# Kernel optimization log

Measured on AMD Instinct MI355X. Metric: run time of the kernel, lower is better.

## Reference

```python
import jax, jax.numpy as jnp
import numpy as np

DIM = 192
HEADS = 8
EPS = 1e-12  # torch F.normalize eps


def _l2norm(t):
    # normalize over last axis, matching torch.nn.functional.normalize
    n = jnp.sqrt(jnp.sum(t * t, axis=-1, keepdims=True))
    return t / jnp.maximum(n, EPS)


def setup_inputs() -> dict:
    key = jax.random.key(0)
    k1, k2, k3, k4 = jax.random.split(key, 4)
    B, C, H, W = 16, DIM, 128, 128
    s = 1.0 / np.sqrt(C)
    return {
        "x": jax.random.normal(k1, (B, C, H, W), dtype=jnp.float32),
        "w_qkv": jax.random.normal(k2, (C, 3 * C), dtype=jnp.float32) * s,
        "w_proj": jax.random.normal(k3, (C, C), dtype=jnp.float32) * s,
        "b_proj": jax.random.normal(k4, (C,), dtype=jnp.float32) * 0.01,
        "temperature": jnp.ones((HEADS, 1, 1), dtype=jnp.float32),
    }


def reference(x, w_qkv, w_proj, b_proj, temperature):
    B, C, H, W = x.shape
    N = H * W
    h = HEADS
    d = C // h
    # [B,C,H,W] -> [B,N,C]
    xt = x.reshape(B, C, N).transpose(0, 2, 1)
    qkv = (xt @ w_qkv).reshape(B, N, 3, h, d)
    qkv = qkv.transpose(2, 0, 3, 1, 4)           # [3,B,h,N,d]
    q, k, v = qkv[0], qkv[1], qkv[2]
    # transpose to channel-as-token: [B,h,d,N]
    q = _l2norm(q.transpose(0, 1, 3, 2))
    k = _l2norm(k.transpose(0, 1, 3, 2))
    v = v.transpose(0, 1, 3, 2)
    # small channel attention matrix [B,h,d,d]
    attn = jnp.einsum("bhdn,bhen->bhde", q, k) * temperature
    attn = jax.nn.softmax(attn, axis=-1)
    out = jnp.einsum("bhde,bhen->bhdn", attn, v)  # [B,h,d,N]
    out = out.transpose(0, 3, 1, 2).reshape(B, N, C)
    out = out @ w_proj + b_proj
    return out.transpose(0, 2, 1).reshape(B, C, H, W)
```

## Files before the change

kernel.cpp:

```cpp
#include <hip/hip_runtime.h>
#include <hip/hip_bf16.h>
#include <math.h>

#define C_DIM 192
#define NTOK 16384
#define NB 16
#define NH 8
#define HD 24
#define EPSN 1e-12f

typedef float f32x4 __attribute__((ext_vector_type(4)));
typedef __bf16 bf16x4 __attribute__((ext_vector_type(4)));
typedef __bf16 bf16x8 __attribute__((ext_vector_type(8)));

__device__ __forceinline__ f32x4 mfma16(bf16x8 a, bf16x8 b, f32x4 c) {
  return __builtin_amdgcn_mfma_f32_16x16x32_bf16(a, b, c, 0, 0, 0);
}

__device__ __forceinline__ bf16x8 cvt8(const float* __restrict__ p) {
  f32x4 a = *(const f32x4*)p;
  f32x4 b = *(const f32x4*)(p + 4);
  bf16x8 r;
  r[0] = (__bf16)a[0]; r[1] = (__bf16)a[1]; r[2] = (__bf16)a[2]; r[3] = (__bf16)a[3];
  r[4] = (__bf16)b[0]; r[5] = (__bf16)b[1]; r[6] = (__bf16)b[2]; r[7] = (__bf16)b[3];
  return r;
}

__global__ __launch_bounds__(256, 2) void k1_gram(const float* __restrict__ x,
                                                  float* __restrict__ gpart,
                                                  int kc) {
  const int b = blockIdx.y, chunk = blockIdx.x;
  const float* xb = x + (size_t)b * C_DIM * NTOK + (size_t)chunk * kc;
  __shared__ __bf16 xsh[2][C_DIM * 32];
  const int t = threadIdx.x;
  const int lane = t & 63, wid = t >> 6;
  const int lrow = lane & 15, loct = lane >> 4;
  const int r0 = (wid >> 1) * 96, c0 = (wid & 1) * 96;
  f32x4 acc[6][6] = {};
  f32x4 stg[6];

#pragma unroll
  for (int it = 0; it < 6; ++it) {
    int idx = it * 256 + t, r = idx >> 3, c8 = idx & 7;
    stg[it] = *(const f32x4*)(xb + (size_t)r * NTOK + 4 * c8);
  }
#pragma unroll
  for (int it = 0; it < 6; ++it) {
    int idx = it * 256 + t, r = idx >> 3, c8 = idx & 7;
    bf16x4 w;
    w[0] = (__bf16)stg[it][0]; w[1] = (__bf16)stg[it][1];
    w[2] = (__bf16)stg[it][2]; w[3] = (__bf16)stg[it][3];
    *(bf16x4*)(&xsh[0][r * 32 + 4 * c8]) = w;
  }
  __syncthreads();

  for (int ks = 0; ks < kc; ks += 32) {
    const int cur = (ks >> 5) & 1;
    const bool more = (ks + 32) < kc;
    if (more) {
#pragma unroll
      for (int it = 0; it < 6; ++it) {
        int idx = it * 256 + t, r = idx >> 3, c8 = idx & 7;
        stg[it] = *(const f32x4*)(xb + (size_t)r * NTOK + ks + 32 + 4 * c8);
      }
    }
    bf16x8 fa[6];
#pragma unroll
    for (int i = 0; i < 6; ++i)
      fa[i] = *(const bf16x8*)(&xsh[cur][(r0 + 16 * i + lrow) * 32 + 8 * loct]);
#pragma unroll
    for (int j = 0; j < 6; ++j) {
      bf16x8 fb = *(const bf16x8*)(&xsh[cur][(c0 + 16 * j + lrow) * 32 + 8 * loct]);
#pragma unroll
      for (int i = 0; i < 6; ++i) acc[i][j] = mfma16(fa[i], fb, acc[i][j]);
    }
    if (more) {
#pragma unroll
      for (int it = 0; it < 6; ++it) {
        int idx = it * 256 + t, r = idx >> 3, c8 = idx & 7;
        bf16x4 w;
        w[0] = (__bf16)stg[it][0]; w[1] = (__bf16)stg[it][1];
        w[2] = (__bf16)stg[it][2]; w[3] = (__bf16)stg[it][3];
        *(bf16x4*)(&xsh[cur ^ 1][r * 32 + 4 * c8]) = w;
      }
    }
    __syncthreads();
  }
  float* gp = gpart + ((size_t)chunk * NB + b) * C_DIM * C_DIM;
#pragma unroll
  for (int i = 0; i < 6; ++i)
#pragma unroll
    for (int j = 0; j < 6; ++j)
#pragma unroll
      for (int e = 0; e < 4; ++e)
        gp[(size_t)(r0 + 16 * i + 4 * loct + e) * C_DIM + (c0 + 16 * j + lrow)] =
            acc[i][j][e];
}

__global__ __launch_bounds__(256) void k2a_reduce(const float* __restrict__ gpart,
                                                  float* __restrict__ G,
                                                  int nchunk) {
  const size_t total = (size_t)NB * C_DIM * C_DIM;
  size_t e0 = ((size_t)blockIdx.x * 256 + threadIdx.x) * 4;
  f32x4 s = {};
  for (int c = 0; c < nchunk; ++c) s += *(const f32x4*)(gpart + c * total + e0);
  *(f32x4*)(G + e0) = s;
}

__global__ __launch_bounds__(256) void k2b1_t(const float* __restrict__ G,
                                              const float* __restrict__ wqkv,
                                              float* __restrict__ Tt) {
  const int b = blockIdx.y, rb = blockIdx.x;
  const int lane = threadIdx.x & 63, wid = threadIdx.x >> 6;
  const int lrow = lane & 15, loct = lane >> 4;
  const float* Gb = G + (size_t)b * C_DIM * C_DIM;
  const int ddA = rb * 64 + wid * 16 + lrow;
  f32x4 acc[12] = {};
  for (int s = 0; s < 6; ++s) {
    bf16x8 fa;
#pragma unroll
    for (int e = 0; e < 8; ++e)
      fa[e] = (__bf16)wqkv[(size_t)(32 * s + 8 * loct + e) * 576 + ddA];
#pragma unroll
    for (int j = 0; j < 12; ++j) {
      bf16x8 fb = cvt8(Gb + (size_t)(16 * j + lrow) * C_DIM + 32 * s + 8 * loct);
      acc[j] = mfma16(fa, fb, acc[j]);
    }
  }
  float* To = Tt + (size_t)b * 384 * C_DIM;
#pragma unroll
  for (int j = 0; j < 12; ++j)
#pragma unroll
    for (int e = 0; e < 4; ++e)
      To[(size_t)(rb * 64 + wid * 16 + 4 * loct + e) * C_DIM + 16 * j + lrow] =
          acc[j][e];
}

__global__ __launch_bounds__(256) void k2b2_attn(const float* __restrict__ Tt,
                                                 const float* __restrict__ wqkv,
                                                 const float* __restrict__ temp,
                                                 float* __restrict__ Yt) {
  const int b = blockIdx.y, h = blockIdx.x;
  __shared__ float SL[32][33];
  __shared__ float qn2L[HD], kn2L[HD];
  const int t = threadIdx.x;
  const int lane = t & 63, wid = t >> 6;
  const int lrow = lane & 15, loct = lane >> 4;
  const float* Tb = Tt + (size_t)b * 384 * C_DIM;
  const int r = wid >> 1, j = wid & 1;
  f32x4 acc = {};
  for (int s = 0; s < 6; ++s) {
    bf16x8 fa = cvt8(Tb + (size_t)(h * HD + 16 * r + lrow) * C_DIM + 32 * s + 8 * loct);
    bf16x8 fb;
#pragma unroll
    for (int e = 0; e < 8; ++e)
      fb[e] = (__bf16)wqkv[(size_t)(32 * s + 8 * loct + e) * 576 + 192 + h * HD +
                           16 * j + lrow];
    acc = mfma16(fa, fb, acc);
  }
#pragma unroll
  for (int e = 0; e < 4; ++e) {
    int d = 16 * r + 4 * loct + e, ee = 16 * j + lrow;
    if (d < HD && ee < HD) SL[d][ee] = acc[e];
  }
  if (t < 48) {
    const int dd = (t < 24) ? t : t - 24;
    const int row = ((t < 24) ? 0 : 192) + h * HD + dd;
    float s = 0.f;
    for (int c = 0; c < C_DIM; ++c)
      s += Tb[(size_t)row * C_DIM + c] * wqkv[(size_t)c * 576 + row];
    if (t < 24) qn2L[dd] = s; else kn2L[dd] = s;
  }
  __syncthreads();
  if (t < HD) {
    const float tp = temp[h];
    float nq = fmaxf(sqrtf(fmaxf(qn2L[t], 0.f)), EPSN);
    float lg[HD];
    float m = -1e30f;
#pragma unroll
    for (int e = 0; e < HD; ++e) {
      float nk = fmaxf(sqrtf(fmaxf(kn2L[e], 0.f)), EPSN);
      lg[e] = SL[t][e] / (nq * nk) * tp;
      m = fmaxf(m, lg[e]);
    }
    float sum = 0.f;
#pragma unroll
    for (int e = 0; e < HD; ++e) { lg[e] = __expf(lg[e] - m); sum += lg[e]; }
    float inv = 1.f / sum;
#pragma unroll
    for (int e = 0; e < HD; ++e) SL[t][e] = lg[e] * inv;
  }
  __syncthreads();
  if (t < C_DIM) {
    float wv[HD];
#pragma unroll
    for (int e = 0; e < HD; ++e)
      wv[e] = wqkv[(size_t)t * 576 + 384 + h * HD + e];
    float* Yo = Yt + ((size_t)b * C_DIM + t) * C_DIM + h * HD;
#pragma unroll
    for (int d = 0; d < HD; ++d) {
      float y = 0.f;
#pragma unroll
      for (int e = 0; e < HD; ++e) y += SL[d][e] * wv[e];
      Yo[d] = y;
    }
  }
}

__global__ __launch_bounds__(256) void k2c_m(const float* __restrict__ wproj,
                                             const float* __restrict__ Yt,
                                             __bf16* __restrict__ M) {
  const int b = blockIdx.y, rb = blockIdx.x;
  const int lane = threadIdx.x & 63, wid = threadIdx.x >> 6;
  const int lrow = lane & 15, loct = lane >> 4;
  const float* Yb = Yt + (size_t)b * C_DIM * C_DIM;
  const int coA = rb * 64 + wid * 16 + lrow;
  f32x4 acc[12] = {};
  for (int s = 0; s < 6; ++s) {
    bf16x8 fa;
#pragma unroll
    for (int e = 0; e < 8; ++e)
      fa[e] = (__bf16)wproj[(size_t)(32 * s + 8 * loct + e) * C_DIM + coA];
#pragma unroll
    for (int j = 0; j < 12; ++j) {
      bf16x8 fb = cvt8(Yb + (size_t)(16 * j + lrow) * C_DIM + 32 * s + 8 * loct);
      acc[j] = mfma16(fa, fb, acc[j]);
    }
  }
  __bf16* Mo = M + (size_t)b * C_DIM * C_DIM;
#pragma unroll
  for (int j = 0; j < 12; ++j)
#pragma unroll
    for (int e = 0; e < 4; ++e)
      Mo[(size_t)(rb * 64 + wid * 16 + 4 * loct + e) * C_DIM + 16 * j + lrow] =
          (__bf16)acc[j][e];
}

__global__ __launch_bounds__(256, 4) void k3_out(const float* __restrict__ x,
                                                 const __bf16* __restrict__ M,
                                                 const float* __restrict__ bproj,
                                                 float* __restrict__ out) {
  const int nt = blockIdx.x, half = blockIdx.y, b = blockIdx.z;
  const int rbase = half * 96;
  __shared__ __bf16 Ml[96 * C_DIM];
  __shared__ float biasL[96];
  const __bf16* Mb = M + (size_t)b * C_DIM * C_DIM + (size_t)rbase * C_DIM;
  for (int i = threadIdx.x; i < 96 * 24; i += 256) {
    int row = i / 24, ch = i % 24;
    bf16x8 v = *(const bf16x8*)(Mb + row * C_DIM + ch * 8);
    *(bf16x8*)(Ml + row * C_DIM + ((ch ^ (row & 7)) * 8)) = v;
  }
  if (threadIdx.x < 96) biasL[threadIdx.x] = bproj[rbase + threadIdx.x];
  __syncthreads();
  const int lane = threadIdx.x & 63, wid = threadIdx.x >> 6;
  const int lrow = lane & 15, loct = lane >> 4;
  const float* xb = x + (size_t)b * C_DIM * NTOK;
  float* ob = out + (size_t)b * C_DIM * NTOK;
  const int n0 = nt * 128 + wid * 32;
  f32x4 acc[6][2] = {};
#pragma unroll
  for (int s = 0; s < 6; ++s) {
    bf16x8 fb0, fb1;
#pragma unroll
    for (int e = 0; e < 8; ++e) {
      size_t rowoff = (size_t)(32 * s + 8 * loct + e) * NTOK;
      fb0[e] = (__bf16)xb[rowoff + n0 + lrow];
      fb1[e] = (__bf16)xb[rowoff + n0 + 16 + lrow];
    }
#pragma unroll
    for (int tt = 0; tt < 6; ++tt) {
      int rowb = 16 * tt + lrow;
      bf16x8 fa = *(const bf16x8*)(Ml + rowb * C_DIM +
                                   (((4 * s + loct) ^ (rowb & 7)) * 8));
      acc[tt][0] = mfma16(fa, fb0, acc[tt][0]);
      acc[tt][1] = mfma16(fa, fb1, acc[tt][1]);
    }
  }
#pragma unroll
  for (int tt = 0; tt < 6; ++tt) {
    const int rw = 16 * tt + 4 * loct;
    f32x4 bias = *(const f32x4*)(biasL + rw);
#pragma unroll
    for (int e = 0; e < 4; ++e) {
      ob[(size_t)(rbase + rw + e) * NTOK + n0 + lrow] = acc[tt][0][e] + bias[e];
      ob[(size_t)(rbase + rw + e) * NTOK + n0 + 16 + lrow] = acc[tt][1][e] + bias[e];
    }
  }
}

extern "C" void kernel_launch(void* const* d_in, const int* in_sizes, int n_in,
                              void* d_out, int out_size, void* d_ws, size_t ws_size,
                              hipStream_t stream) {
  const float* x = (const float*)d_in[0];
  const float* wqkv = (const float*)d_in[1];
  const float* wproj = (const float*)d_in[2];
  const float* bproj = (const float*)d_in[3];
  const float* temp = (const float*)d_in[4];
  float* out = (float*)d_out;

  const size_t GSZ = (size_t)NB * C_DIM * C_DIM;
  const size_t TSZ = (size_t)NB * 384 * C_DIM;
  int nchunk = 32;
  while (nchunk > 1 &&
         ((size_t)nchunk * GSZ + GSZ + TSZ + GSZ + GSZ) * 4 > ws_size)
    nchunk >>= 1;
  float* wsf = (float*)d_ws;
  float* gpart = wsf;
  float* G = gpart + (size_t)nchunk * GSZ;
  float* Tt = G + GSZ;
  float* Yt = Tt + TSZ;
  __bf16* M = (__bf16*)(Yt + GSZ);

  k1_gram<<<dim3(nchunk, NB), 256, 0, stream>>>(x, gpart, NTOK / nchunk);
  k2a_reduce<<<dim3(576), 256, 0, stream>>>(gpart, G, nchunk);
  k2b1_t<<<dim3(6, NB), 256, 0, stream>>>(G, wqkv, Tt);
  k2b2_attn<<<dim3(NH, NB), 256, 0, stream>>>(Tt, wqkv, temp, Yt);
  k2c_m<<<dim3(3, NB), 256, 0, stream>>>(wproj, Yt, M);
  k3_out<<<dim3(128, 2, NB), 256, 0, stream>>>(x, M, bproj, out);
}
```

Baseline: 232.6 us.

## Pad gram LDS rows and restructure output GEMM to read x once

The gram kernel's shared tile row stride is padded from 32 to 40 bf16 elements, which should cut LDS bank conflicts on the MFMA fragment loads. The output kernel is rebuilt so each block covers all 192 output channels for 64 tokens. Previously two blocks each covered half the channels, so x was read twice. M fragments are now read straight from global memory instead of being staged in LDS. The next x slice is prefetched into registers, and the epilogue goes through an LDS transpose to issue 16-byte coalesced stores. This trades heavier M traffic through the cache, and more registers, for half the x reads and wider writes.

New measurement: 275.5 us. 18.4% more time.

```diff
diff --git a/kernel.cpp b/kernel.cpp
--- a/kernel.cpp
+++ b/kernel.cpp
@@ -31,7 +31,7 @@
                                                   int kc) {
   const int b = blockIdx.y, chunk = blockIdx.x;
   const float* xb = x + (size_t)b * C_DIM * NTOK + (size_t)chunk * kc;
-  __shared__ __bf16 xsh[2][C_DIM * 32];
+  __shared__ __bf16 xsh[2][C_DIM * 40];
   const int t = threadIdx.x;
   const int lane = t & 63, wid = t >> 6;
   const int lrow = lane & 15, loct = lane >> 4;
@@ -50,7 +50,7 @@
     bf16x4 w;
     w[0] = (__bf16)stg[it][0]; w[1] = (__bf16)stg[it][1];
     w[2] = (__bf16)stg[it][2]; w[3] = (__bf16)stg[it][3];
-    *(bf16x4*)(&xsh[0][r * 32 + 4 * c8]) = w;
+    *(bf16x4*)(&xsh[0][r * 40 + 4 * c8]) = w;
   }
   __syncthreads();
 
@@ -67,10 +67,10 @@
     bf16x8 fa[6];
 #pragma unroll
     for (int i = 0; i < 6; ++i)
-      fa[i] = *(const bf16x8*)(&xsh[cur][(r0 + 16 * i + lrow) * 32 + 8 * loct]);
+      fa[i] = *(const bf16x8*)(&xsh[cur][(r0 + 16 * i + lrow) * 40 + 8 * loct]);
 #pragma unroll
     for (int j = 0; j < 6; ++j) {
-      bf16x8 fb = *(const bf16x8*)(&xsh[cur][(c0 + 16 * j + lrow) * 32 + 8 * loct]);
+      bf16x8 fb = *(const bf16x8*)(&xsh[cur][(c0 + 16 * j + lrow) * 40 + 8 * loct]);
 #pragma unroll
       for (int i = 0; i < 6; ++i) acc[i][j] = mfma16(fa[i], fb, acc[i][j]);
     }
@@ -81,7 +81,7 @@
         bf16x4 w;
         w[0] = (__bf16)stg[it][0]; w[1] = (__bf16)stg[it][1];
         w[2] = (__bf16)stg[it][2]; w[3] = (__bf16)stg[it][3];
-        *(bf16x4*)(&xsh[cur ^ 1][r * 32 + 4 * c8]) = w;
+        *(bf16x4*)(&xsh[cur ^ 1][r * 40 + 4 * c8]) = w;
       }
     }
     __syncthreads();
@@ -240,50 +240,70 @@
                                                  const __bf16* __restrict__ M,
                                                  const float* __restrict__ bproj,
                                                  float* __restrict__ out) {
-  const int nt = blockIdx.x, half = blockIdx.y, b = blockIdx.z;
-  const int rbase = half * 96;
-  __shared__ __bf16 Ml[96 * C_DIM];
-  __shared__ float biasL[96];
-  const __bf16* Mb = M + (size_t)b * C_DIM * C_DIM + (size_t)rbase * C_DIM;
-  for (int i = threadIdx.x; i < 96 * 24; i += 256) {
-    int row = i / 24, ch = i % 24;
-    bf16x8 v = *(const bf16x8*)(Mb + row * C_DIM + ch * 8);
-    *(bf16x8*)(Ml + row * C_DIM + ((ch ^ (row & 7)) * 8)) = v;
-  }
-  if (threadIdx.x < 96) biasL[threadIdx.x] = bproj[rbase + threadIdx.x];
+  const int nt = blockIdx.x, b = blockIdx.y;
+  __shared__ float epi[4][16 * 68];
+  __shared__ float biasL[C_DIM];
+  const int t = threadIdx.x;
+  const int lane = t & 63, w = t >> 6;
+  const int lrow = lane & 15, loct = lane >> 4;
+  if (t < C_DIM) biasL[t] = bproj[t];
+
+  const float* xb = x + (size_t)b * C_DIM * NTOK + nt * 64;
+  const __bf16* Mb = M + (size_t)b * C_DIM * C_DIM;
+  float* ob = out + (size_t)b * C_DIM * NTOK + nt * 64;
+
+  f32x4 acc[3][4] = {};
+  float xs[4][8];
+#pragma unroll
+  for (int nf = 0; nf < 4; ++nf)
+#pragma unroll
+    for (int e = 0; e < 8; ++e)
+      xs[nf][e] = xb[(size_t)(8 * loct + e) * NTOK + 16 * nf + lrow];
+
+  for (int s = 0; s < 6; ++s) {
+    bf16x8 fb[4];
+#pragma unroll
+    for (int nf = 0; nf < 4; ++nf)
+#pragma unroll
+      for (int e = 0; e < 8; ++e)
+        fb[nf][e] = (__bf16)xs[nf][e];
+    if (s < 5) {
+#pragma unroll
+      for (int nf = 0; nf < 4; ++nf)
+#pragma unroll
+        for (int e = 0; e < 8; ++e)
+          xs[nf][e] =
+              xb[(size_t)(32 * (s + 1) + 8 * loct + e) * NTOK + 16 * nf + lrow];
+    }
+    bf16x8 fa[3];
+#pragma unroll
+    for (int tt = 0; tt < 3; ++tt)
+      fa[tt] = *(const bf16x8*)(Mb + (size_t)(48 * w + 16 * tt + lrow) * C_DIM +
+                                32 * s + 8 * loct);
+#pragma unroll
+    for (int tt = 0; tt < 3; ++tt)
+#pragma unroll
+      for (int nf = 0; nf < 4; ++nf)
+        acc[tt][nf] = mfma16(fa[tt], fb[nf], acc[tt][nf]);
+  }
+
   __syncthreads();
-  const int lane = threadIdx.x & 63, wid = threadIdx.x >> 6;
-  const int lrow = lane & 15, loct = lane >> 4;
-  const float* xb = x + (size_t)b * C_DIM * NTOK;
-  float* ob = out + (size_t)b * C_DIM * NTOK;
-  const int n0 = nt * 128 + wid * 32;
-  f32x4 acc[6][2] = {};
-#pragma unroll
-  for (int s = 0; s < 6; ++s) {
-    bf16x8 fb0, fb1;
-#pragma unroll
-    for (int e = 0; e < 8; ++e) {
-      size_t rowoff = (size_t)(32 * s + 8 * loct + e) * NTOK;
-      fb0[e] = (__bf16)xb[rowoff + n0 + lrow];
-      fb1[e] = (__bf16)xb[rowoff + n0 + 16 + lrow];
-    }
-#pragma unroll
-    for (int tt = 0; tt < 6; ++tt) {
-      int rowb = 16 * tt + lrow;
-      bf16x8 fa = *(const bf16x8*)(Ml + rowb * C_DIM +
-                                   (((4 * s + loct) ^ (rowb & 7)) * 8));
-      acc[tt][0] = mfma16(fa, fb0, acc[tt][0]);
-      acc[tt][1] = mfma16(fa, fb1, acc[tt][1]);
-    }
-  }
-#pragma unroll
-  for (int tt = 0; tt < 6; ++tt) {
-    const int rw = 16 * tt + 4 * loct;
-    f32x4 bias = *(const f32x4*)(biasL + rw);
-#pragma unroll
-    for (int e = 0; e < 4; ++e) {
-      ob[(size_t)(rbase + rw + e) * NTOK + n0 + lrow] = acc[tt][0][e] + bias[e];
-      ob[(size_t)(rbase + rw + e) * NTOK + n0 + 16 + lrow] = acc[tt][1][e] + bias[e];
+  float* epi_w = epi[w];
+#pragma unroll
+  for (int tt = 0; tt < 3; ++tt) {
+#pragma unroll
+    for (int nf = 0; nf < 4; ++nf)
+#pragma unroll
+      for (int e = 0; e < 4; ++e) {
+        int rr = 4 * loct + e;
+        epi_w[rr * 68 + 16 * nf + lrow] =
+            acc[tt][nf][e] + biasL[48 * w + 16 * tt + rr];
+      }
+#pragma unroll
+    for (int h = 0; h < 4; ++h) {
+      int rr = 4 * h + loct;
+      f32x4 v = *(const f32x4*)(epi_w + rr * 68 + 4 * lrow);
+      *(f32x4*)(ob + (size_t)(48 * w + 16 * tt + rr) * NTOK + 4 * lrow) = v;
     }
   }
 }
@@ -316,5 +336,5 @@
   k2b1_t<<<dim3(6, NB), 256, 0, stream>>>(G, wqkv, Tt);
   k2b2_attn<<<dim3(NH, NB), 256, 0, stream>>>(Tt, wqkv, temp, Yt);
   k2c_m<<<dim3(3, NB), 256, 0, stream>>>(wproj, Yt, M);
-  k3_out<<<dim3(128, 2, NB), 256, 0, stream>>>(x, M, bproj, out);
-}
+  k3_out<<<dim3(NTOK / 64, NB), 256, 0, stream>>>(x, M, bproj, out);
+}
```

## Pad Gram LDS tiles, prefetch x, and stage output through LDS for wide stores

Applied to the files above, without the earlier changes.

The Gram kernel's shared-memory row stride goes from 32 to 40 bf16 elements to reduce LDS bank conflicts on fragment reads. The output kernel now loads the next slice of x into registers while the current slice runs through the MFMAs, a simple software pipeline. Its epilogue writes each wave's accumulators plus bias into LDS with a padded stride of 33 floats. It then reads them back as float4 so global stores are 128-bit and contiguous along tokens. The f32x4 LDS reads at a 33-float stride are not 16-byte aligned, which may be split into narrower accesses or cost extra.

New measurement: 229.0 us. About the same (-1.6%).

```diff
diff --git a/kernel.cpp b/kernel.cpp
--- a/kernel.cpp
+++ b/kernel.cpp
@@ -31,7 +31,7 @@
                                                   int kc) {
   const int b = blockIdx.y, chunk = blockIdx.x;
   const float* xb = x + (size_t)b * C_DIM * NTOK + (size_t)chunk * kc;
-  __shared__ __bf16 xsh[2][C_DIM * 32];
+  __shared__ __bf16 xsh[2][C_DIM * 40];
   const int t = threadIdx.x;
   const int lane = t & 63, wid = t >> 6;
   const int lrow = lane & 15, loct = lane >> 4;
@@ -50,7 +50,7 @@
     bf16x4 w;
     w[0] = (__bf16)stg[it][0]; w[1] = (__bf16)stg[it][1];
     w[2] = (__bf16)stg[it][2]; w[3] = (__bf16)stg[it][3];
-    *(bf16x4*)(&xsh[0][r * 32 + 4 * c8]) = w;
+    *(bf16x4*)(&xsh[0][r * 40 + 4 * c8]) = w;
   }
   __syncthreads();
 
@@ -67,10 +67,10 @@
     bf16x8 fa[6];
 #pragma unroll
     for (int i = 0; i < 6; ++i)
-      fa[i] = *(const bf16x8*)(&xsh[cur][(r0 + 16 * i + lrow) * 32 + 8 * loct]);
+      fa[i] = *(const bf16x8*)(&xsh[cur][(r0 + 16 * i + lrow) * 40 + 8 * loct]);
 #pragma unroll
     for (int j = 0; j < 6; ++j) {
-      bf16x8 fb = *(const bf16x8*)(&xsh[cur][(c0 + 16 * j + lrow) * 32 + 8 * loct]);
+      bf16x8 fb = *(const bf16x8*)(&xsh[cur][(c0 + 16 * j + lrow) * 40 + 8 * loct]);
 #pragma unroll
       for (int i = 0; i < 6; ++i) acc[i][j] = mfma16(fa[i], fb, acc[i][j]);
     }
@@ -81,7 +81,7 @@
         bf16x4 w;
         w[0] = (__bf16)stg[it][0]; w[1] = (__bf16)stg[it][1];
         w[2] = (__bf16)stg[it][2]; w[3] = (__bf16)stg[it][3];
-        *(bf16x4*)(&xsh[cur ^ 1][r * 32 + 4 * c8]) = w;
+        *(bf16x4*)(&xsh[cur ^ 1][r * 40 + 4 * c8]) = w;
       }
     }
     __syncthreads();
@@ -244,46 +244,73 @@
   const int rbase = half * 96;
   __shared__ __bf16 Ml[96 * C_DIM];
   __shared__ float biasL[96];
+  const int t = threadIdx.x;
+  const int lane = t & 63, w = t >> 6;
+  const int lrow = lane & 15, loct = lane >> 4;
+
   const __bf16* Mb = M + (size_t)b * C_DIM * C_DIM + (size_t)rbase * C_DIM;
-  for (int i = threadIdx.x; i < 96 * 24; i += 256) {
+  for (int i = t; i < 96 * 24; i += 256) {
     int row = i / 24, ch = i % 24;
     bf16x8 v = *(const bf16x8*)(Mb + row * C_DIM + ch * 8);
     *(bf16x8*)(Ml + row * C_DIM + ((ch ^ (row & 7)) * 8)) = v;
   }
-  if (threadIdx.x < 96) biasL[threadIdx.x] = bproj[rbase + threadIdx.x];
-  __syncthreads();
-  const int lane = threadIdx.x & 63, wid = threadIdx.x >> 6;
-  const int lrow = lane & 15, loct = lane >> 4;
+  if (t < 96) biasL[t] = bproj[rbase + t];
+  __syncthreads();
+
   const float* xb = x + (size_t)b * C_DIM * NTOK;
   float* ob = out + (size_t)b * C_DIM * NTOK;
-  const int n0 = nt * 128 + wid * 32;
+  const int n0 = nt * 128 + w * 32;
+
   f32x4 acc[6][2] = {};
-#pragma unroll
+  float xs[2][8];
+#pragma unroll
+  for (int nf = 0; nf < 2; ++nf)
+#pragma unroll
+    for (int e = 0; e < 8; ++e)
+      xs[nf][e] = xb[(size_t)(8 * loct + e) * NTOK + n0 + 16 * nf + lrow];
+
   for (int s = 0; s < 6; ++s) {
-    bf16x8 fb0, fb1;
-#pragma unroll
-    for (int e = 0; e < 8; ++e) {
-      size_t rowoff = (size_t)(32 * s + 8 * loct + e) * NTOK;
-      fb0[e] = (__bf16)xb[rowoff + n0 + lrow];
-      fb1[e] = (__bf16)xb[rowoff + n0 + 16 + lrow];
+    bf16x8 fb[2];
+#pragma unroll
+    for (int nf = 0; nf < 2; ++nf)
+#pragma unroll
+      for (int e = 0; e < 8; ++e)
+        fb[nf][e] = (__bf16)xs[nf][e];
+    if (s < 5) {
+#pragma unroll
+      for (int nf = 0; nf < 2; ++nf)
+#pragma unroll
+        for (int e = 0; e < 8; ++e)
+          xs[nf][e] =
+              xb[(size_t)(32 * (s + 1) + 8 * loct + e) * NTOK + n0 + 16 * nf + lrow];
     }
 #pragma unroll
     for (int tt = 0; tt < 6; ++tt) {
       int rowb = 16 * tt + lrow;
       bf16x8 fa = *(const bf16x8*)(Ml + rowb * C_DIM +
                                    (((4 * s + loct) ^ (rowb & 7)) * 8));
-      acc[tt][0] = mfma16(fa, fb0, acc[tt][0]);
-      acc[tt][1] = mfma16(fa, fb1, acc[tt][1]);
-    }
-  }
+      acc[tt][0] = mfma16(fa, fb[0], acc[tt][0]);
+      acc[tt][1] = mfma16(fa, fb[1], acc[tt][1]);
+    }
+  }
+
+  __syncthreads();
+  float* epi_w = (float*)Ml + w * 544;
 #pragma unroll
   for (int tt = 0; tt < 6; ++tt) {
-    const int rw = 16 * tt + 4 * loct;
-    f32x4 bias = *(const f32x4*)(biasL + rw);
-#pragma unroll
-    for (int e = 0; e < 4; ++e) {
-      ob[(size_t)(rbase + rw + e) * NTOK + n0 + lrow] = acc[tt][0][e] + bias[e];
-      ob[(size_t)(rbase + rw + e) * NTOK + n0 + 16 + lrow] = acc[tt][1][e] + bias[e];
+#pragma unroll
+    for (int nf = 0; nf < 2; ++nf)
+#pragma unroll
+      for (int e = 0; e < 4; ++e) {
+        int rr = 4 * loct + e;
+        epi_w[rr * 33 + 16 * nf + lrow] =
+            acc[tt][nf][e] + biasL[16 * tt + rr];
+      }
+#pragma unroll
+    for (int h = 0; h < 2; ++h) {
+      int rr = 8 * h + 2 * loct + (lrow >> 3);
+      f32x4 v = *(const f32x4*)(epi_w + rr * 33 + 4 * (lrow & 7));
+      *(f32x4*)(ob + (size_t)(rbase + 16 * tt + rr) * NTOK + n0 + 4 * (lrow & 7)) = v;
     }
   }
 }
```
